# Optimization experiments

Measured on AMD Instinct MI355X. Metric: run time of the kernel, lower is better.

The kernel has to match this reference:

```python
import jax, jax.numpy as jnp
import numpy as np

SEQ, B, H, NP, HN = 2048, 2, 2048, 16, 128
SCALE = 1.0 / 11.313708498984761  # 1/sqrt(128), hardcoded in the source baddbmm


def setup_inputs() -> dict:
    key = jax.random.key(0)
    k1, k2, k3 = jax.random.split(key, 3)
    return {
        "hidden_states": jax.random.normal(k1, (SEQ, B, H), dtype=jnp.float32),
        "w_qkv": jax.random.normal(k2, (3 * H, H), dtype=jnp.float32) * 0.02,
        "w_out": jax.random.normal(k3, (H, H), dtype=jnp.float32) * 0.02,
    }


def reference(hidden_states, w_qkv, w_out):
    s, b, h = hidden_states.shape
    # QKV projection (column-parallel linear, no bias): [s, b, 3h]
    qkv = hidden_states @ w_qkv.T
    # [s, b, np, 3*hn] then split (num_query_groups == num_heads)
    qkv = qkv.reshape(s, b, NP, 3 * HN)
    q, k, v = qkv[..., :HN], qkv[..., HN:2 * HN], qkv[..., 2 * HN:]
    # baddbmm QK^T with alpha = 1/sqrt(128): scores [b, np, sq, sk]
    scores = jnp.einsum("sbnh,tbnh->bnst", q, k) * SCALE
    # scale_t == 1 then plain softmax (fallback path; no mask applied)
    prob = jax.nn.softmax(scores, axis=-1)
    # context: bmm(prob, V) -> [sq, b, np, hn] -> [sq, b, h]
    ctx = jnp.einsum("bnst,tbnh->sbnh", prob, v).reshape(s, b, h)
    # row-parallel output linear (no bias)
    return ctx @ w_out.T
```

## Files before the change

kernel.cpp:

```cpp
#include <hip/hip_runtime.h>
#include <stdint.h>

#define SEQ 2048
#define BATCH 2
#define HID 2048
#define NHEADS 16
#define HDIM 128
#define QKV_LD 6144
#define SCALE_F 0.08838834764831845f
#define LOG2E_F 1.4426950408889634f

typedef unsigned short u16;
using bf16x8 = __attribute__((ext_vector_type(8))) short;
using f32x4  = __attribute__((ext_vector_type(4))) float;

__device__ inline u16 f2bf(float f) {
  union { float f; uint32_t u; } c; c.f = f;
  uint32_t u = c.u;
  uint32_t r = (u + 0x7fffu + ((u >> 16) & 1u)) >> 16;
  return (u16)r;
}

__device__ inline void gl_lds16(const u16* g, u16* l) {
  __builtin_amdgcn_global_load_lds((const __attribute__((address_space(1))) void*)g,
                                   (__attribute__((address_space(3))) void*)l,
                                   16, 0, 0);
}

__global__ void cvt_f32_bf16(const float* __restrict__ in, u16* __restrict__ out, int n4) {
  int i = blockIdx.x * blockDim.x + threadIdx.x;
  if (i >= n4) return;
  float4 v = ((const float4*)in)[i];
  ushort4 o;
  o.x = f2bf(v.x); o.y = f2bf(v.y); o.z = f2bf(v.z); o.w = f2bf(v.w);
  ((ushort4*)out)[i] = o;
}

__global__ void cvt_wqkv_scaled(const float* __restrict__ in, u16* __restrict__ out, int n4) {
  int i = blockIdx.x * blockDim.x + threadIdx.x;
  if (i >= n4) return;
  const int f = i >> 9;
  const float sc = ((f % 384) < 128) ? SCALE_F : 1.0f;
  float4 v = ((const float4*)in)[i];
  ushort4 o;
  o.x = f2bf(v.x * sc); o.y = f2bf(v.y * sc); o.z = f2bf(v.z * sc); o.w = f2bf(v.w * sc);
  ((ushort4*)out)[i] = o;
}

template<bool OUT_BF16>
__global__ __launch_bounds__(256)
void gemm_bt(const u16* __restrict__ A, const u16* __restrict__ Bw,
             void* __restrict__ Cout, int M, int N, int K) {
  __shared__ __align__(16) u16 As[128 * 32];
  __shared__ __align__(16) u16 Bs[128 * 32];
  const int bm = blockIdx.x, bn = blockIdx.y;
  const int tid = threadIdx.x;
  const int wave = tid >> 6, lane = tid & 63;
  const int quad = lane >> 4, l16 = lane & 15;
  const int wm = (wave >> 1) * 64, wn = (wave & 1) * 64;
  f32x4 acc[4][4] = {};

  const u16* Ablk = A + (size_t)(bm * 128) * K;
  const u16* Bblk = Bw + (size_t)(bn * 128) * K;

  for (int k0 = 0; k0 < K; k0 += 32) {
    __syncthreads();
    #pragma unroll
    for (int p = 0; p < 2; ++p) {
      int chunk = p * 256 + tid;
      int r = chunk >> 2, cc = chunk & 3;
      gl_lds16(Ablk + (size_t)r * K + k0 + cc * 8, As + (p * 256 + wave * 64) * 8);
      gl_lds16(Bblk + (size_t)r * K + k0 + cc * 8, Bs + (p * 256 + wave * 64) * 8);
    }
    __syncthreads();
    bf16x8 af[4], bfr[4];
    #pragma unroll
    for (int mt = 0; mt < 4; ++mt)
      af[mt] = *(const bf16x8*)&As[(wm + mt * 16 + l16) * 32 + quad * 8];
    #pragma unroll
    for (int nt = 0; nt < 4; ++nt)
      bfr[nt] = *(const bf16x8*)&Bs[(wn + nt * 16 + l16) * 32 + quad * 8];
    #pragma unroll
    for (int mt = 0; mt < 4; ++mt)
      #pragma unroll
      for (int nt = 0; nt < 4; ++nt)
        acc[mt][nt] = __builtin_amdgcn_mfma_f32_16x16x32_bf16(af[mt], bfr[nt], acc[mt][nt], 0, 0, 0);
  }

  #pragma unroll
  for (int mt = 0; mt < 4; ++mt) {
    #pragma unroll
    for (int nt = 0; nt < 4; ++nt) {
      #pragma unroll
      for (int r = 0; r < 4; ++r) {
        int row = bm * 128 + wm + mt * 16 + quad * 4 + r;
        int col = bn * 128 + wn + nt * 16 + l16;
        float v = acc[mt][nt][r];
        if (OUT_BF16) ((u16*)Cout)[(size_t)row * N + col] = f2bf(v);
        else          ((float*)Cout)[(size_t)row * N + col] = v;
      }
    }
  }
}

__global__ __launch_bounds__(256)
void transpose_v(const u16* __restrict__ qkv, u16* __restrict__ vt) {
  __shared__ u16 Vs[64][132];
  const int st = blockIdx.x, head = blockIdx.y, b = blockIdx.z;
  const int s0 = st * 64;
  const int t = threadIdx.x;
  {
    const int r = t >> 2, c0 = (t & 3) * 32;
    const u16* src = qkv + ((size_t)(s0 + r) * BATCH + b) * QKV_LD + head * 384 + 256 + c0;
    #pragma unroll
    for (int j = 0; j < 4; ++j)
      *(uint4*)&Vs[r][c0 + j * 8] = *(const uint4*)(src + j * 8);
  }
  __syncthreads();
  {
    const int hd = t & 127, sc = (t >> 7) * 32;
    u16 tmp[32];
    #pragma unroll
    for (int j = 0; j < 32; ++j) tmp[j] = Vs[sc + j][hd];
    u16* dst = vt + ((size_t)(b * NHEADS + head) * HDIM + hd) * SEQ + s0 + sc;
    #pragma unroll
    for (int j = 0; j < 4; ++j)
      *(uint4*)&dst[j * 8] = *(const uint4*)&tmp[j * 8];
  }
}

__global__ __launch_bounds__(256, 2)
void attn(const u16* __restrict__ qkv, const u16* __restrict__ vt_g, u16* __restrict__ ctx) {
  const int qt = blockIdx.x, head = blockIdx.y, b = blockIdx.z;
  const int q0 = qt * 128;
  __shared__ __align__(16) u16 Ks[64 * 128];
  __shared__ __align__(16) u16 Vt[144 * 64];
  __shared__ __align__(16) u16 Ps[128 * 72];
  const int tid = threadIdx.x;
  const int wave = tid >> 6, lane = tid & 63;
  const int quad = lane >> 4, l16 = lane & 15;

  const u16* qkv_bh = qkv + (size_t)b * QKV_LD + head * 384;
  const u16* vt = vt_g + (size_t)(b * NHEADS + head) * HDIM * SEQ;

  if (tid < 128) {
    const int row = 128 + (tid >> 3), c = tid & 7;
    const u16 v = (row == 128) ? (u16)0x3F80 : (u16)0;
    ushort4 q4; q4.x = v; q4.y = v; q4.z = v; q4.w = v;
    *(ushort4*)&Vt[(row * 8 + c) * 8] = q4;
    *(ushort4*)&Vt[(row * 8 + c) * 8 + 4] = q4;
  }

  bf16x8 qf[2][4];
  #pragma unroll
  for (int h = 0; h < 2; ++h) {
    __syncthreads();
    #pragma unroll
    for (int p = 0; p < 4; ++p) {
      int j = p * 256 + tid;
      int r = j >> 4, cs = j & 15, c = cs ^ (r & 7);
      gl_lds16(qkv_bh + (size_t)(q0 + h * 64 + r) * (BATCH * QKV_LD) + c * 8,
               Ks + (p * 256 + wave * 64) * 8);
    }
    __syncthreads();
    if ((wave >> 1) == h) {
      #pragma unroll
      for (int mt = 0; mt < 2; ++mt)
        #pragma unroll
        for (int ks = 0; ks < 4; ++ks) {
          int row = (wave & 1) * 32 + mt * 16 + l16;
          int cc = (ks * 4 + quad) ^ (row & 7);
          qf[mt][ks] = *(const bf16x8*)&Ks[(row * 16 + cc) * 8];
        }
    }
  }

  f32x4 o[2][9] = {};

  for (int kt = 0; kt < SEQ; kt += 64) {
    __syncthreads();
    #pragma unroll
    for (int p = 0; p < 4; ++p) {
      int j = p * 256 + tid;
      int r = j >> 4, cs = j & 15, c = cs ^ (r & 7);
      gl_lds16(qkv_bh + (size_t)(kt + r) * (BATCH * QKV_LD) + 128 + c * 8,
               Ks + (p * 256 + wave * 64) * 8);
    }
    #pragma unroll
    for (int p = 0; p < 4; ++p) {
      int j = p * 256 + tid;
      int hd = j >> 3, cs = j & 7, c = cs ^ (hd & 7);
      gl_lds16(vt + (size_t)hd * SEQ + kt + c * 8,
               Vt + (p * 256 + wave * 64) * 8);
    }
    __syncthreads();

    f32x4 s[2][4] = {};
    #pragma unroll
    for (int ks = 0; ks < 4; ++ks) {
      bf16x8 bk[4];
      #pragma unroll
      for (int nt = 0; nt < 4; ++nt) {
        int row = nt * 16 + l16;
        int cc = (ks * 4 + quad) ^ (row & 7);
        bk[nt] = *(const bf16x8*)&Ks[(row * 16 + cc) * 8];
      }
      #pragma unroll
      for (int mt = 0; mt < 2; ++mt)
        #pragma unroll
        for (int nt = 0; nt < 4; ++nt)
          s[mt][nt] = __builtin_amdgcn_mfma_f32_16x16x32_bf16(qf[mt][ks], bk[nt], s[mt][nt], 0, 0, 0);
    }

    #pragma unroll
    for (int mt = 0; mt < 2; ++mt)
      #pragma unroll
      for (int r = 0; r < 4; ++r) {
        const int prow = (wave * 32 + mt * 16 + quad * 4 + r) * 72;
        #pragma unroll
        for (int nt = 0; nt < 4; ++nt) {
          float ex = __builtin_amdgcn_exp2f(s[mt][nt][r] * LOG2E_F);
          union { float f; uint32_t u; } cv; cv.f = ex;
          Ps[prow + nt * 16 + l16] = (u16)(cv.u >> 16);
        }
      }

    #pragma unroll
    for (int ks = 0; ks < 2; ++ks) {
      bf16x8 ap[2], bv[9];
      #pragma unroll
      for (int mt = 0; mt < 2; ++mt)
        ap[mt] = *(const bf16x8*)&Ps[(wave * 32 + mt * 16 + l16) * 72 + ks * 32 + quad * 8];
      #pragma unroll
      for (int nt = 0; nt < 9; ++nt) {
        int hd = nt * 16 + l16;
        int cc = (ks * 4 + quad) ^ (hd & 7);
        bv[nt] = *(const bf16x8*)&Vt[(hd * 8 + cc) * 8];
      }
      #pragma unroll
      for (int mt = 0; mt < 2; ++mt)
        #pragma unroll
        for (int nt = 0; nt < 9; ++nt)
          o[mt][nt] = __builtin_amdgcn_mfma_f32_16x16x32_bf16(ap[mt], bv[nt], o[mt][nt], 0, 0, 0);
    }
  }

  #pragma unroll
  for (int mt = 0; mt < 2; ++mt)
    #pragma unroll
    for (int r = 0; r < 4; ++r) {
      const float lv = __shfl(o[mt][8][r], lane & 48);
      const float inv_l = 1.0f / lv;
      const int srow = q0 + wave * 32 + mt * 16 + quad * 4 + r;
      u16* dst = ctx + ((size_t)srow * BATCH + b) * HID + head * HDIM;
      #pragma unroll
      for (int nt = 0; nt < 8; ++nt)
        dst[nt * 16 + l16] = f2bf(o[mt][nt][r] * inv_l);
    }
}

extern "C" void kernel_launch(void* const* d_in, const int* in_sizes, int n_in,
                              void* d_out, int out_size, void* d_ws, size_t ws_size,
                              hipStream_t stream) {
  const float* hs   = (const float*)d_in[0];
  const float* wqkv = (const float*)d_in[1];
  const float* wout = (const float*)d_in[2];
  float* out = (float*)d_out;
  char* ws = (char*)d_ws;

  u16* hs_bf   = (u16*)(ws);
  u16* wqkv_bf = (u16*)(ws + 16777216);
  u16* wout_bf = (u16*)(ws + 41943040);
  u16* qkv_bf  = (u16*)(ws + 50331648);
  u16* ctx_bf  = (u16*)(ws + 100663296);
  u16* vt_bf   = hs_bf;

  cvt_f32_bf16<<<8192, 256, 0, stream>>>(hs, hs_bf, 2097152);
  cvt_wqkv_scaled<<<12288, 256, 0, stream>>>(wqkv, wqkv_bf, 3145728);
  cvt_f32_bf16<<<4096, 256, 0, stream>>>(wout, wout_bf, 1048576);

  gemm_bt<true><<<dim3(32, 48), 256, 0, stream>>>(hs_bf, wqkv_bf, qkv_bf, 4096, 6144, 2048);

  transpose_v<<<dim3(32, NHEADS, BATCH), 256, 0, stream>>>(qkv_bf, vt_bf);

  attn<<<dim3(16, NHEADS, BATCH), 256, 0, stream>>>(qkv_bf, vt_bf, ctx_bf);

  gemm_bt<false><<<dim3(32, 16), 256, 0, stream>>>(ctx_bf, wout_bf, out, 4096, 2048, 2048);
}
```

Baseline: 431.3 us.

## Merge fp32->bf16 converts into one kernel; widen GEMM K-tile with XOR-swizzled LDS

The three conversion kernels become a single launch that writes into the contiguous workspace region, relying on the hs/wqkv/wout buffers being laid out back to back. The GEMM K step doubles from 32 to 64, and a column XOR swizzle on the LDS layout avoids bank conflicts on the fragment reads. This halves the number of barrier pairs per K and cuts launch overhead, at the cost of twice the LDS per block.

```diff
diff --git a/kernel.cpp b/kernel.cpp
--- a/kernel.cpp
+++ b/kernel.cpp
@@ -27,32 +27,30 @@
                                    16, 0, 0);
 }
 
-__global__ void cvt_f32_bf16(const float* __restrict__ in, u16* __restrict__ out, int n4) {
+__global__ void cvt_all(const float* __restrict__ hs, const float* __restrict__ wqkv,
+                        const float* __restrict__ wout, u16* __restrict__ ws_out) {
   int i = blockIdx.x * blockDim.x + threadIdx.x;
-  if (i >= n4) return;
-  float4 v = ((const float4*)in)[i];
-  ushort4 o;
-  o.x = f2bf(v.x); o.y = f2bf(v.y); o.z = f2bf(v.z); o.w = f2bf(v.w);
-  ((ushort4*)out)[i] = o;
-}
-
-__global__ void cvt_wqkv_scaled(const float* __restrict__ in, u16* __restrict__ out, int n4) {
-  int i = blockIdx.x * blockDim.x + threadIdx.x;
-  if (i >= n4) return;
-  const int f = i >> 9;
-  const float sc = ((f % 384) < 128) ? SCALE_F : 1.0f;
-  float4 v = ((const float4*)in)[i];
+  const float* src;
+  int j;
+  float sc = 1.0f;
+  if (i < 2097152) { src = hs; j = i; }
+  else if (i < 5242880) {
+    j = i - 2097152; src = wqkv;
+    const int f = j >> 9;
+    if ((f % 384) < 128) sc = SCALE_F;
+  } else { j = i - 5242880; src = wout; }
+  float4 v = ((const float4*)src)[j];
   ushort4 o;
   o.x = f2bf(v.x * sc); o.y = f2bf(v.y * sc); o.z = f2bf(v.z * sc); o.w = f2bf(v.w * sc);
-  ((ushort4*)out)[i] = o;
+  ((ushort4*)ws_out)[i] = o;
 }
 
 template<bool OUT_BF16>
 __global__ __launch_bounds__(256)
 void gemm_bt(const u16* __restrict__ A, const u16* __restrict__ Bw,
              void* __restrict__ Cout, int M, int N, int K) {
-  __shared__ __align__(16) u16 As[128 * 32];
-  __shared__ __align__(16) u16 Bs[128 * 32];
+  __shared__ __align__(16) u16 As[128 * 64];
+  __shared__ __align__(16) u16 Bs[128 * 64];
   const int bm = blockIdx.x, bn = blockIdx.y;
   const int tid = threadIdx.x;
   const int wave = tid >> 6, lane = tid & 63;
@@ -63,28 +61,37 @@
   const u16* Ablk = A + (size_t)(bm * 128) * K;
   const u16* Bblk = Bw + (size_t)(bn * 128) * K;
 
-  for (int k0 = 0; k0 < K; k0 += 32) {
-    __syncthreads();
-    #pragma unroll
-    for (int p = 0; p < 2; ++p) {
-      int chunk = p * 256 + tid;
-      int r = chunk >> 2, cc = chunk & 3;
-      gl_lds16(Ablk + (size_t)r * K + k0 + cc * 8, As + (p * 256 + wave * 64) * 8);
-      gl_lds16(Bblk + (size_t)r * K + k0 + cc * 8, Bs + (p * 256 + wave * 64) * 8);
-    }
-    __syncthreads();
-    bf16x8 af[4], bfr[4];
-    #pragma unroll
-    for (int mt = 0; mt < 4; ++mt)
-      af[mt] = *(const bf16x8*)&As[(wm + mt * 16 + l16) * 32 + quad * 8];
-    #pragma unroll
-    for (int nt = 0; nt < 4; ++nt)
-      bfr[nt] = *(const bf16x8*)&Bs[(wn + nt * 16 + l16) * 32 + quad * 8];
-    #pragma unroll
-    for (int mt = 0; mt < 4; ++mt)
-      #pragma unroll
-      for (int nt = 0; nt < 4; ++nt)
-        acc[mt][nt] = __builtin_amdgcn_mfma_f32_16x16x32_bf16(af[mt], bfr[nt], acc[mt][nt], 0, 0, 0);
+  for (int k0 = 0; k0 < K; k0 += 64) {
+    __syncthreads();
+    #pragma unroll
+    for (int p = 0; p < 4; ++p) {
+      int j = p * 256 + tid;
+      int r = j >> 3, cs = j & 7, c = cs ^ (r & 7);
+      gl_lds16(Ablk + (size_t)r * K + k0 + c * 8, As + (p * 256 + wave * 64) * 8);
+      gl_lds16(Bblk + (size_t)r * K + k0 + c * 8, Bs + (p * 256 + wave * 64) * 8);
+    }
+    __syncthreads();
+    #pragma unroll
+    for (int ks = 0; ks < 2; ++ks) {
+      bf16x8 af[4], bfr[4];
+      #pragma unroll
+      for (int mt = 0; mt < 4; ++mt) {
+        int row = wm + mt * 16 + l16;
+        int cc = (ks * 4 + quad) ^ (row & 7);
+        af[mt] = *(const bf16x8*)&As[(row * 8 + cc) * 8];
+      }
+      #pragma unroll
+      for (int nt = 0; nt < 4; ++nt) {
+        int row = wn + nt * 16 + l16;
+        int cc = (ks * 4 + quad) ^ (row & 7);
+        bfr[nt] = *(const bf16x8*)&Bs[(row * 8 + cc) * 8];
+      }
+      #pragma unroll
+      for (int mt = 0; mt < 4; ++mt)
+        #pragma unroll
+        for (int nt = 0; nt < 4; ++nt)
+          acc[mt][nt] = __builtin_amdgcn_mfma_f32_16x16x32_bf16(af[mt], bfr[nt], acc[mt][nt], 0, 0, 0);
+    }
   }
 
   #pragma unroll
@@ -275,9 +282,7 @@
   u16* ctx_bf  = (u16*)(ws + 100663296);
   u16* vt_bf   = hs_bf;
 
-  cvt_f32_bf16<<<8192, 256, 0, stream>>>(hs, hs_bf, 2097152);
-  cvt_wqkv_scaled<<<12288, 256, 0, stream>>>(wqkv, wqkv_bf, 3145728);
-  cvt_f32_bf16<<<4096, 256, 0, stream>>>(wout, wout_bf, 1048576);
+  cvt_all<<<24576, 256, 0, stream>>>(hs, wqkv, wout, (u16*)ws);
 
   gemm_bt<true><<<dim3(32, 48), 256, 0, stream>>>(hs_bf, wqkv_bf, qkv_bf, 4096, 6144, 2048);
 
```

Result: faster. 384.7 us (-10.8%).
